# Performance work log

Hardware: AMD Instinct MI355X
Metric: run time of the kernel (lower is better)

The kernel has to match this reference:

```python
import jax, jax.numpy as jnp
import numpy as np

N = 50000        # nodes
E = 800000       # edges (avg degree 16)
D_IN = 64
D_HID = 128      # 2 * out_dim
D_OUT = 64


def setup_inputs() -> dict:
    key = jax.random.key(0)
    ks = jax.random.split(key, 6)
    x = jax.random.normal(ks[0], (N, D_IN), dtype=jnp.float32)
    edge_index = jax.random.randint(ks[1], (2, E), 0, N, dtype=jnp.int32)
    # Glorot-style init like PyG GCNConv
    W1 = jax.random.normal(ks[2], (D_IN, D_HID), dtype=jnp.float32) / np.sqrt(D_IN)
    b1 = jnp.zeros((D_HID,), dtype=jnp.float32)
    W2 = jax.random.normal(ks[3], (D_HID, D_OUT), dtype=jnp.float32) / np.sqrt(D_HID)
    b2 = jnp.zeros((D_OUT,), dtype=jnp.float32)
    return {"x": x, "edge_index": edge_index, "W1": W1, "b1": b1, "W2": W2, "b2": b2}


def _gcn_norm(edge_index, num_nodes):
    # PyG GCNConv default: add self-loops, symmetric normalization D^-1/2 A_hat D^-1/2
    loop = jnp.arange(num_nodes, dtype=edge_index.dtype)
    src = jnp.concatenate([edge_index[0], loop])
    dst = jnp.concatenate([edge_index[1], loop])
    deg = jax.ops.segment_sum(jnp.ones_like(dst, dtype=jnp.float32), dst,
                              num_segments=num_nodes)
    dinv = jnp.where(deg > 0, jax.lax.rsqrt(deg), 0.0)
    norm = dinv[src] * dinv[dst]  # [E+N]
    return src, dst, norm


def _gcn_conv(x, W, b, src, dst, norm, num_nodes):
    h = x @ W                                      # [N, F_out]
    msg = h[src] * norm[:, None]                   # gather + scale, [E+N, F_out]
    out = jax.ops.segment_sum(msg, dst, num_segments=num_nodes)  # scatter-add
    return out + b


def reference(x, edge_index, W1, b1, W2, b2):
    num_nodes = x.shape[0]
    src, dst, norm = _gcn_norm(edge_index, num_nodes)
    h = _gcn_conv(x, W1, b1, src, dst, norm, num_nodes)
    h = jax.nn.relu(h)
    node_emb = _gcn_conv(h, W2, b2, src, dst, norm, num_nodes)
    return node_emb
```

## Files before the change

### kernel.cpp

```cpp
#include <hip/hip_runtime.h>

typedef unsigned short u16;
typedef unsigned int u32;

typedef __attribute__((ext_vector_type(8))) short bf16x8;
typedef __attribute__((ext_vector_type(4))) float f32x4;

#define BSH 8
#define CAP 5120
#define OVFCAP 8192
#define CHUNK 2048

__device__ __forceinline__ float bf2f(u16 u) {
    return __uint_as_float(((u32)u) << 16);
}
__device__ __forceinline__ u16 f2bf(float f) {
    u32 x = __float_as_uint(f);
    return (u16)((x + 0x7fffu + ((x >> 16) & 1u)) >> 16);
}

__device__ __forceinline__ bool block_isbf(const u16* __restrict__ x, float* sflag) {
    int tid = threadIdx.x;
    if (tid < 64) {
        u16 v = x[tid * 2];
        u32 ex = (v >> 7) & 0xFFu;
        unsigned long long m = __ballot(ex >= 90u && ex <= 140u);
        if (tid == 0) *sflag = (m == ~0ull) ? 1.0f : 0.0f;
    }
    __syncthreads();
    return *sflag != 0.0f;
}

__device__ __forceinline__ void gather_accum(
    const u32* __restrict__ fl, const u16* __restrict__ csr,
    int s0, int s1, int lane, float& ax, float& ay) {
    int deg = s1 - s0;
    for (int base = 0; base < deg; base += 32) {
        int m = min(deg - base, 32);
        int idx = 0;
        if (lane < m) idx = (int)csr[s0 + base + lane];
        int j = 0;
        for (; j + 8 <= m; j += 8) {
            u32 wv[8];
#pragma unroll
            for (int u = 0; u < 8; u++) {
                int sv = __shfl(idx, j + u, 32);
                wv[u] = fl[(size_t)sv * 32];
            }
#pragma unroll
            for (int u = 0; u < 8; u++) {
                ax += bf2f((u16)(wv[u] & 0xFFFFu));
                ay += bf2f((u16)(wv[u] >> 16));
            }
        }
        for (; j + 4 <= m; j += 4) {
            u32 wv[4];
#pragma unroll
            for (int u = 0; u < 4; u++) {
                int sv = __shfl(idx, j + u, 32);
                wv[u] = fl[(size_t)sv * 32];
            }
#pragma unroll
            for (int u = 0; u < 4; u++) {
                ax += bf2f((u16)(wv[u] & 0xFFFFu));
                ay += bf2f((u16)(wv[u] >> 16));
            }
        }
        for (; j < m; j++) {
            int sv = __shfl(idx, j, 32);
            u32 wa = fl[(size_t)sv * 32];
            ax += bf2f((u16)(wa & 0xFFFFu));
            ay += bf2f((u16)(wa >> 16));
        }
    }
}

__global__ __launch_bounds__(256) void k_binA2(
    const int* __restrict__ src, const int* __restrict__ dst,
    int* __restrict__ gcur, u32* __restrict__ staging,
    u32* __restrict__ ovf, int* __restrict__ ovfcur, int E) {
    __shared__ int hcnt[256];
    __shared__ int hbase[256];
    const int tid = threadIdx.x;
    const int e0 = blockIdx.x * CHUNK;
    const int e1 = min(e0 + CHUNK, E);
    hcnt[tid] = 0;
    __syncthreads();
    for (int e = e0 + tid; e < e1; e += 256)
        atomicAdd(&hcnt[dst[e] >> BSH], 1);
    __syncthreads();
    {
        int c = hcnt[tid];
        hbase[tid] = (c > 0) ? atomicAdd(&gcur[tid], c) : 0;
        hcnt[tid] = 0;
    }
    __syncthreads();
    for (int e = e0 + tid; e < e1; e += 256) {
        int d = dst[e];
        int s = src[e];
        int b = d >> BSH;
        int r = atomicAdd(&hcnt[b], 1);
        int p = hbase[b] + r;
        if (p < CAP) {
            staging[(size_t)b * CAP + p] = (u32)s | ((u32)(d & 255) << 16);
        } else {
            int q = atomicAdd(ovfcur, 1);
            if (q < OVFCAP) ovf[q] = (u32)s | ((u32)d << 16);
        }
    }
}

__global__ __launch_bounds__(256) void k_bucket(
    const u32* __restrict__ staging, const int* __restrict__ gcur,
    const u32* __restrict__ ovf, const int* __restrict__ ovfcur,
    int* __restrict__ row_start, float* __restrict__ dinv,
    u16* __restrict__ csr, int nbuck,
    const void* __restrict__ W1, const void* __restrict__ b1,
    const void* __restrict__ W2, const void* __restrict__ b2,
    u16* __restrict__ wc,
    const void* __restrict__ x, u16* __restrict__ gxt, int N, int E) {
    __shared__ float sflag;
    __shared__ int hcnt[256];
    __shared__ int hscan[256];
    __shared__ int hcur[256];
    __shared__ int sred[256];
    __shared__ int sbase;
    __shared__ float sdinv[256];
    const int bid = blockIdx.x;
    const int tid = threadIdx.x;
    bool isbf = block_isbf((const u16*)x, &sflag);

    if (bid < nbuck) {
        const int b = bid;
        const int used = min(gcur[b], CAP);
        const u32* st = staging + (size_t)b * CAP;
        const int no = min(ovfcur[0], OVFCAP);
        sred[tid] = (tid < b) ? gcur[tid] : 0;
        hcnt[tid] = 0;
        __syncthreads();
        for (int s = 128; s > 0; s >>= 1) {
            if (tid < s) sred[tid] += sred[tid + s];
            __syncthreads();
        }
        if (tid == 0) sbase = sred[0];
        for (int i = tid; i < used; i += 256)
            atomicAdd(&hcnt[st[i] >> 16], 1);
        for (int i = tid; i < no; i += 256) {
            u32 pk = ovf[i];
            int d = (int)(pk >> 16);
            if ((d >> BSH) == b) atomicAdd(&hcnt[d & 255], 1);
        }
        __syncthreads();
        int v = hcnt[tid];
        hscan[tid] = v;
        __syncthreads();
        for (int s = 1; s < 256; s <<= 1) {
            int t = (tid >= s) ? hscan[tid - s] : 0;
            __syncthreads();
            hscan[tid] += t;
            __syncthreads();
        }
        int excl = hscan[tid] - v;
        hcur[tid] = excl;
        int base = sbase;
        float dv = rsqrtf((float)(v + 1));
        sdinv[tid] = dv;
        int node = (b << BSH) + tid;
        if (node < N) {
            row_start[node] = base + excl;
            dinv[node] = dv;
        }
        if (b == 0 && tid == 0) row_start[N] = E;
        __syncthreads();
        for (int i = tid; i < used; i += 256) {
            u32 pk = st[i];
            int r = atomicAdd(&hcur[pk >> 16], 1);
            csr[base + r] = (u16)(pk & 0xFFFFu);
        }
        for (int i = tid; i < no; i += 256) {
            u32 pk = ovf[i];
            int d = (int)(pk >> 16);
            if ((d >> BSH) == b) {
                int r = atomicAdd(&hcur[d & 255], 1);
                csr[base + r] = (u16)(pk & 0xFFFFu);
            }
        }
        const int row0 = b << BSH;
        for (int i = tid; i < 256 * 16; i += 256) {
            int rl = i >> 4;
            int node2 = row0 + rl;
            if (node2 >= N) break;
            int q = i & 15;
            size_t idx = (size_t)node2 * 16 + q;
            float di = sdinv[rl];
            float4 vv;
            if (isbf) {
                ushort4 u = ((const ushort4*)x)[idx];
                vv.x = bf2f(u.x); vv.y = bf2f(u.y); vv.z = bf2f(u.z); vv.w = bf2f(u.w);
            } else {
                vv = ((const float4*)x)[idx];
            }
            ushort4 o;
            o.x = f2bf(vv.x * di); o.y = f2bf(vv.y * di);
            o.z = f2bf(vv.z * di); o.w = f2bf(vv.w * di);
            ((ushort4*)gxt)[idx] = o;
        }
    } else {
        int cb = bid - nbuck;
        for (int i = cb * 256 + tid; i < 16576; i += 17 * 256) {
            const void* s; int off;
            if (i < 8192)       { int nn = i >> 6, k = i & 63;  s = W1; off = k * 128 + nn; }
            else if (i < 16384) { int j = i - 8192; int nn = j >> 7, k = j & 127; s = W2; off = k * 64 + nn; }
            else if (i < 16512) { s = b1; off = i - 16384; }
            else                { s = b2; off = i - 16512; }
            wc[i] = isbf ? ((const u16*)s)[off] : f2bf(((const float*)s)[off]);
        }
    }
}

template<bool FINAL>
__global__ __launch_bounds__(256) void k_gather(
    const u32* __restrict__ feat, const int* __restrict__ row_start,
    const u16* __restrict__ csr, const float* __restrict__ dinv,
    const u16* __restrict__ b2c, const void* __restrict__ xdet,
    void* __restrict__ outp, int n) {
    __shared__ float sflag;
    bool isbf = true;
    if (FINAL) isbf = block_isbf((const u16*)xdet, &sflag);
    int t = blockIdx.x * 256 + threadIdx.x;
    int d = t >> 5;
    int lane = t & 31;
    if (d >= n) return;
    const u32* fl = feat + lane;
    u32 w = fl[(size_t)d * 32];
    float ax = bf2f((u16)(w & 0xFFFFu));
    float ay = bf2f((u16)(w >> 16));
    gather_accum(fl, csr, row_start[d], row_start[d + 1], lane, ax, ay);
    if (FINAL) {
        float di = dinv[d];
        ax = ax * di + bf2f(b2c[2 * lane + 0]);
        ay = ay * di + bf2f(b2c[2 * lane + 1]);
        if (isbf) {
            u32 o = (u32)f2bf(ax) | ((u32)f2bf(ay) << 16);
            ((u32*)outp)[(size_t)d * 32 + lane] = o;
        } else {
            ((float2*)outp)[(size_t)d * 32 + lane] = make_float2(ax, ay);
        }
    } else {
        u32 o = (u32)f2bf(ax) | ((u32)f2bf(ay) << 16);
        ((u32*)outp)[(size_t)d * 32 + lane] = o;
    }
}

__global__ __launch_bounds__(256) void k_mlp(
    const u16* __restrict__ accin, const u16* __restrict__ wc,
    const float* __restrict__ dinv, u16* outb, int n) {
    __shared__ __align__(16) u16 As[32 * 72];
    __shared__ __align__(16) u16 W1t[128 * 72];
    __shared__ __align__(16) u16 W2t[64 * 136];
    __shared__ __align__(16) u16 Hs[32 * 136];
    __shared__ float b1s[128];
    __shared__ float dvs[32];
    const int tid = threadIdx.x;
    const int row0 = blockIdx.x * 32;

    if (tid < 32) {
        int r = row0 + tid;
        dvs[tid] = (r < n) ? dinv[r] : 0.f;
    } else if (tid < 160) {
        b1s[tid - 32] = bf2f(wc[16384 + tid - 32]);
    }
    for (int i = tid; i < 1024; i += 256) {
        int r = i >> 5, kk = i & 31;
        int row = row0 + r;
        u32 v = 0;
        if (row < n) {
            u32 g = ((const u32*)accin)[(size_t)row * 32 + kk];
            float di = dinv[row];
            u16 lo = f2bf(bf2f((u16)(g & 0xFFFFu)) * di);
            u16 hi = f2bf(bf2f((u16)(g >> 16)) * di);
            v = (u32)lo | ((u32)hi << 16);
        }
        *(u32*)&As[r * 72 + kk * 2] = v;
    }
    for (int i = tid; i < 4096; i += 256) {
        int nn = i >> 5, kk = i & 31;
        *(u32*)&W1t[nn * 72 + kk * 2] = ((const u32*)wc)[i];
    }
    for (int i = tid; i < 4096; i += 256) {
        int nn = i >> 6, kk = i & 63;
        *(u32*)&W2t[nn * 136 + kk * 2] = ((const u32*)wc)[4096 + i];
    }
    __syncthreads();

    const int wave = tid >> 6;
    const int lane = tid & 63;
    const int q = lane >> 4;
    const int ln = lane & 15;

    bf16x8 a[2][2];
#pragma unroll
    for (int mt = 0; mt < 2; mt++)
#pragma unroll
        for (int ks = 0; ks < 2; ks++)
            a[mt][ks] = *(const bf16x8*)&As[(mt * 16 + ln) * 72 + ks * 32 + q * 8];

    f32x4 c1[2][2];
#pragma unroll
    for (int ntl = 0; ntl < 2; ntl++)
#pragma unroll
        for (int mt = 0; mt < 2; mt++) c1[ntl][mt] = (f32x4){0.f, 0.f, 0.f, 0.f};

#pragma unroll
    for (int ntl = 0; ntl < 2; ntl++) {
        int nt = wave * 2 + ntl;
        bf16x8 b0 = *(const bf16x8*)&W1t[(nt * 16 + ln) * 72 + 0 + q * 8];
        bf16x8 b1f = *(const bf16x8*)&W1t[(nt * 16 + ln) * 72 + 32 + q * 8];
#pragma unroll
        for (int mt = 0; mt < 2; mt++) {
            c1[ntl][mt] = __builtin_amdgcn_mfma_f32_16x16x32_bf16(a[mt][0], b0, c1[ntl][mt], 0, 0, 0);
            c1[ntl][mt] = __builtin_amdgcn_mfma_f32_16x16x32_bf16(a[mt][1], b1f, c1[ntl][mt], 0, 0, 0);
        }
    }
#pragma unroll
    for (int ntl = 0; ntl < 2; ntl++) {
        int col = (wave * 2 + ntl) * 16 + ln;
        float bb = b1s[col];
#pragma unroll
        for (int mt = 0; mt < 2; mt++)
#pragma unroll
            for (int r = 0; r < 4; r++) {
                int hrow = mt * 16 + q * 4 + r;
                Hs[hrow * 136 + col] = f2bf(fmaxf(c1[ntl][mt][r] + bb, 0.f));
            }
    }
    __syncthreads();

    f32x4 c2[2];
    c2[0] = (f32x4){0.f, 0.f, 0.f, 0.f};
    c2[1] = (f32x4){0.f, 0.f, 0.f, 0.f};
#pragma unroll
    for (int ks = 0; ks < 4; ks++) {
        bf16x8 bb = *(const bf16x8*)&W2t[(wave * 16 + ln) * 136 + ks * 32 + q * 8];
#pragma unroll
        for (int mt = 0; mt < 2; mt++) {
            bf16x8 aa = *(const bf16x8*)&Hs[(mt * 16 + ln) * 136 + ks * 32 + q * 8];
            c2[mt] = __builtin_amdgcn_mfma_f32_16x16x32_bf16(aa, bb, c2[mt], 0, 0, 0);
        }
    }
#pragma unroll
    for (int mt = 0; mt < 2; mt++)
#pragma unroll
        for (int r = 0; r < 4; r++) {
            int rloc = mt * 16 + q * 4 + r;
            int row = row0 + rloc;
            if (row < n) {
                int col = wave * 16 + ln;
                outb[(size_t)row * 64 + col] = f2bf(c2[mt][r] * dvs[rloc]);
            }
        }
}

extern "C" void kernel_launch(void* const* d_in, const int* in_sizes, int n_in,
                              void* d_out, int out_size, void* d_ws, size_t ws_size,
                              hipStream_t stream) {
    const void* x  = d_in[0];
    const int* ei  = (const int*)d_in[1];
    const void* W1 = d_in[2];
    const void* b1 = d_in[3];
    const void* W2 = d_in[4];
    const void* b2 = d_in[5];

    const int N = in_sizes[0] / 64;
    const int E = in_sizes[1] / 2;
    const int* src = ei;
    const int* dst = ei + E;

    float* ws = (float*)d_ws;
    const int NP = ((N + 64) + 63) & ~63;
    float* dinv    = ws;
    int* gcur      = (int*)(ws + NP);
    int* ovfcur    = gcur + 256;
    int* row_start = gcur + 320;
    u32* ovf       = (u32*)(row_start + ((N + 64) & ~63));
    u16* csr       = (u16*)(ovf + OVFCAP);
    u16* wc        = (u16*)(((size_t)(csr + E) + 255) & ~(size_t)255);
    u16* bufB      = (u16*)(((size_t)(wc + 16576) + 255) & ~(size_t)255);
    u32* staging   = (u32*)bufB;
    u16* gxt       = (u16*)d_out;

    const int gth = (N * 32 + 255) / 256;
    const int nbuck = (N + 255) >> BSH;
    const int binB = (E + CHUNK - 1) / CHUNK;
    dim3 blk(256);

    hipMemsetAsync(gcur, 0, 320 * sizeof(int), stream);
    k_binA2<<<dim3(binB), blk, 0, stream>>>(src, dst, gcur, staging, ovf, ovfcur, E);
    k_bucket<<<dim3(nbuck + 17), blk, 0, stream>>>(staging, gcur, ovf, ovfcur,
                                                   row_start, dinv, csr, nbuck,
                                                   W1, b1, W2, b2, wc, x, gxt, N, E);
    k_gather<false><<<dim3(gth), blk, 0, stream>>>((const u32*)gxt, row_start, csr,
                                                   dinv, wc + 16512, x, bufB, N);
    k_mlp<<<dim3((N + 31) / 32), blk, 0, stream>>>((const u16*)bufB, wc, dinv, bufB, N);
    k_gather<true><<<dim3(gth), blk, 0, stream>>>((const u32*)bufB, row_start, csr,
                                                  dinv, wc + 16512, x, d_out, N);
}
```

Before: 158.9 us.

## Gather with 8 lanes per node using 16-byte vector loads

Both gather kernels now assign 8 lanes per destination node instead of 32, and each lane loads a uint4 (8 bf16 values) per neighbor instead of a single u32. This cuts the number of load instructions and lets one wavefront work on 8 nodes at once, which should help latency hiding on the irregular gathers. The tail handling and output stores are rewritten to match the wider vectors. In exchange each lane holds more accumulator registers and does more serial work per node.

```diff
diff --git a/kernel.cpp b/kernel.cpp
--- a/kernel.cpp
+++ b/kernel.cpp
@@ -31,48 +31,11 @@
     return *sflag != 0.0f;
 }
 
-__device__ __forceinline__ void gather_accum(
-    const u32* __restrict__ fl, const u16* __restrict__ csr,
-    int s0, int s1, int lane, float& ax, float& ay) {
-    int deg = s1 - s0;
-    for (int base = 0; base < deg; base += 32) {
-        int m = min(deg - base, 32);
-        int idx = 0;
-        if (lane < m) idx = (int)csr[s0 + base + lane];
-        int j = 0;
-        for (; j + 8 <= m; j += 8) {
-            u32 wv[8];
-#pragma unroll
-            for (int u = 0; u < 8; u++) {
-                int sv = __shfl(idx, j + u, 32);
-                wv[u] = fl[(size_t)sv * 32];
-            }
-#pragma unroll
-            for (int u = 0; u < 8; u++) {
-                ax += bf2f((u16)(wv[u] & 0xFFFFu));
-                ay += bf2f((u16)(wv[u] >> 16));
-            }
-        }
-        for (; j + 4 <= m; j += 4) {
-            u32 wv[4];
-#pragma unroll
-            for (int u = 0; u < 4; u++) {
-                int sv = __shfl(idx, j + u, 32);
-                wv[u] = fl[(size_t)sv * 32];
-            }
-#pragma unroll
-            for (int u = 0; u < 4; u++) {
-                ax += bf2f((u16)(wv[u] & 0xFFFFu));
-                ay += bf2f((u16)(wv[u] >> 16));
-            }
-        }
-        for (; j < m; j++) {
-            int sv = __shfl(idx, j, 32);
-            u32 wa = fl[(size_t)sv * 32];
-            ax += bf2f((u16)(wa & 0xFFFFu));
-            ay += bf2f((u16)(wa >> 16));
-        }
-    }
+__device__ __forceinline__ void acc8(uint4 w, float* a) {
+    a[0] += bf2f((u16)(w.x & 0xFFFFu)); a[1] += bf2f((u16)(w.x >> 16));
+    a[2] += bf2f((u16)(w.y & 0xFFFFu)); a[3] += bf2f((u16)(w.y >> 16));
+    a[4] += bf2f((u16)(w.z & 0xFFFFu)); a[5] += bf2f((u16)(w.z >> 16));
+    a[6] += bf2f((u16)(w.w & 0xFFFFu)); a[7] += bf2f((u16)(w.w >> 16));
 }
 
 __global__ __launch_bounds__(256) void k_binA2(
@@ -220,7 +183,7 @@
 
 template<bool FINAL>
 __global__ __launch_bounds__(256) void k_gather(
-    const u32* __restrict__ feat, const int* __restrict__ row_start,
+    const uint4* __restrict__ feat, const int* __restrict__ row_start,
     const u16* __restrict__ csr, const float* __restrict__ dinv,
     const u16* __restrict__ b2c, const void* __restrict__ xdet,
     void* __restrict__ outp, int n) {
@@ -228,27 +191,66 @@
     bool isbf = true;
     if (FINAL) isbf = block_isbf((const u16*)xdet, &sflag);
     int t = blockIdx.x * 256 + threadIdx.x;
-    int d = t >> 5;
-    int lane = t & 31;
+    int d = t >> 3;
+    int lane = t & 7;
     if (d >= n) return;
-    const u32* fl = feat + lane;
-    u32 w = fl[(size_t)d * 32];
-    float ax = bf2f((u16)(w & 0xFFFFu));
-    float ay = bf2f((u16)(w >> 16));
-    gather_accum(fl, csr, row_start[d], row_start[d + 1], lane, ax, ay);
+    const uint4* fl = feat + lane;
+    float a[8];
+    {
+        uint4 w = fl[(size_t)d * 8];
+        a[0] = bf2f((u16)(w.x & 0xFFFFu)); a[1] = bf2f((u16)(w.x >> 16));
+        a[2] = bf2f((u16)(w.y & 0xFFFFu)); a[3] = bf2f((u16)(w.y >> 16));
+        a[4] = bf2f((u16)(w.z & 0xFFFFu)); a[5] = bf2f((u16)(w.z >> 16));
+        a[6] = bf2f((u16)(w.w & 0xFFFFu)); a[7] = bf2f((u16)(w.w >> 16));
+    }
+    int s0 = row_start[d], s1 = row_start[d + 1];
+    int deg = s1 - s0;
+    int j = s0;
+    int end8 = s0 + (deg & ~7);
+    for (; j < end8; j += 8) {
+        int idx = (int)csr[j + lane];
+        uint4 wv[8];
+#pragma unroll
+        for (int u = 0; u < 8; u++) {
+            int sv = __shfl(idx, u, 8);
+            wv[u] = fl[(size_t)sv * 8];
+        }
+#pragma unroll
+        for (int u = 0; u < 8; u++) acc8(wv[u], a);
+    }
+    int rem = s1 - j;
+    if (rem > 0) {
+        int idx = (lane < rem) ? (int)csr[j + lane] : 0;
+        for (int u = 0; u < rem; u++) {
+            int sv = __shfl(idx, u, 8);
+            uint4 wv = fl[(size_t)sv * 8];
+            acc8(wv, a);
+        }
+    }
     if (FINAL) {
         float di = dinv[d];
-        ax = ax * di + bf2f(b2c[2 * lane + 0]);
-        ay = ay * di + bf2f(b2c[2 * lane + 1]);
+#pragma unroll
+        for (int u = 0; u < 8; u++)
+            a[u] = a[u] * di + bf2f(b2c[8 * lane + u]);
         if (isbf) {
-            u32 o = (u32)f2bf(ax) | ((u32)f2bf(ay) << 16);
-            ((u32*)outp)[(size_t)d * 32 + lane] = o;
+            uint4 o;
+            o.x = (u32)f2bf(a[0]) | ((u32)f2bf(a[1]) << 16);
+            o.y = (u32)f2bf(a[2]) | ((u32)f2bf(a[3]) << 16);
+            o.z = (u32)f2bf(a[4]) | ((u32)f2bf(a[5]) << 16);
+            o.w = (u32)f2bf(a[6]) | ((u32)f2bf(a[7]) << 16);
+            ((uint4*)outp)[(size_t)d * 8 + lane] = o;
         } else {
-            ((float2*)outp)[(size_t)d * 32 + lane] = make_float2(ax, ay);
+            float4* op = (float4*)outp;
+            op[(size_t)d * 16 + 2 * lane]     = make_float4(a[0], a[1], a[2], a[3]);
+            op[(size_t)d * 16 + 2 * lane + 1] = make_float4(a[4], a[5], a[6], a[7]);
         }
     } else {
-        u32 o = (u32)f2bf(ax) | ((u32)f2bf(ay) << 16);
-        ((u32*)outp)[(size_t)d * 32 + lane] = o;
+        uint4 o;
+        o.x = (u32)f2bf(a[0]) | ((u32)f2bf(a[1]) << 16);
+        o.y = (u32)f2bf(a[2]) | ((u32)f2bf(a[3]) << 16);
+        o.z = (u32)f2bf(a[4]) | ((u32)f2bf(a[5]) << 16);
+        o.w = (u32)f2bf(a[6]) | ((u32)f2bf(a[7]) << 16);
+        ((uint4*)outp)[(size_t)d * 8 + lane] = o;
     }
 }
 
@@ -389,7 +391,7 @@
     u32* staging   = (u32*)bufB;
     u16* gxt       = (u16*)d_out;
 
-    const int gth = (N * 32 + 255) / 256;
+    const int gth = (N * 8 + 255) / 256;
     const int nbuck = (N + 255) >> BSH;
     const int binB = (E + CHUNK - 1) / CHUNK;
     dim3 blk(256);
@@ -399,9 +401,9 @@
     k_bucket<<<dim3(nbuck + 17), blk, 0, stream>>>(staging, gcur, ovf, ovfcur,
                                                    row_start, dinv, csr, nbuck,
                                                    W1, b1, W2, b2, wc, x, gxt, N, E);
-    k_gather<false><<<dim3(gth), blk, 0, stream>>>((const u32*)gxt, row_start, csr,
+    k_gather<false><<<dim3(gth), blk, 0, stream>>>((const uint4*)gxt, row_start, csr,
                                                    dinv, wc + 16512, x, bufB, N);
     k_mlp<<<dim3((N + 31) / 32), blk, 0, stream>>>((const u16*)bufB, wc, dinv, bufB, N);
-    k_gather<true><<<dim3(gth), blk, 0, stream>>>((const u32*)bufB, row_start, csr,
+    k_gather<true><<<dim3(gth), blk, 0, stream>>>((const uint4*)bufB, row_start, csr,
                                                   dinv, wc + 16512, x, d_out, N);
 }
```

After: 160.5 us. About the same (+1.0%).
